# Kernel tuning notes

Hardware: AMD Instinct MI355X
Metric: run time of the kernel (lower is better)

The kernel has to match this reference:

```python
import jax, jax.numpy as jnp
import numpy as np

B, S, D, H = 4, 2048, 512, 8
DEPTH = D // H
EPS = 1e-6

def setup_inputs() -> dict:
    key = jax.random.key(0)
    ks = jax.random.split(key, 5)
    scale = 1.0 / np.sqrt(D)
    return {
        "x": jax.random.normal(ks[0], (B, S, D), dtype=jnp.float32),
        "wq": jax.random.normal(ks[1], (D, D), dtype=jnp.float32) * scale,
        "wk": jax.random.normal(ks[2], (D, D), dtype=jnp.float32) * scale,
        "wv": jax.random.normal(ks[3], (D, D), dtype=jnp.float32) * scale,
        "wo": jax.random.normal(ks[4], (D, D), dtype=jnp.float32) * scale,
        "bo": jnp.zeros((D,), dtype=jnp.float32),
        "gamma": jnp.ones((D,), dtype=jnp.float32),
        "beta": jnp.zeros((D,), dtype=jnp.float32),
    }

def _split_heads(t):
    # [B,S,D] -> [B,H,S,depth]
    return t.reshape(B, S, H, DEPTH).transpose(0, 2, 1, 3)

def reference(x, wq, wk, wv, wo, bo, gamma, beta):
    q = _split_heads(x @ wq)
    k = _split_heads(x @ wk)
    v = _split_heads(x @ wv)
    logits = jnp.einsum("bhqd,bhkd->bhqk", q, k) / jnp.sqrt(jnp.float32(DEPTH))
    attn = jax.nn.softmax(logits, axis=-1)  # dropout is identity at inference
    ctx = jnp.einsum("bhqk,bhkd->bhqd", attn, v)
    ctx = ctx.transpose(0, 2, 1, 3).reshape(B, S, D)
    out = ctx @ wo + bo
    resid = x + out  # output dropout identity at inference
    mu = jnp.mean(resid, axis=-1, keepdims=True)
    var = jnp.mean(jnp.square(resid - mu), axis=-1, keepdims=True)
    return (resid - mu) / jnp.sqrt(var + EPS) * gamma + beta
```

## Files before the change

### kernel.cpp

```cpp
#include <hip/hip_runtime.h>
#include <hip/hip_bf16.h>

typedef __attribute__((ext_vector_type(8))) short short8;
typedef __attribute__((ext_vector_type(4))) float f32x4;

constexpr int B_ = 4, S_ = 2048, D_ = 512, H_ = 8, DP_ = 64;
constexpr int M_ = B_ * S_;

__device__ __forceinline__ unsigned short f2b(float f) {
    __hip_bfloat16 h = __float2bfloat16(f);
    return *reinterpret_cast<unsigned short*>(&h);
}

__device__ __forceinline__ void gload_lds16(const unsigned short* g, unsigned short* l) {
    __builtin_amdgcn_global_load_lds((const __attribute__((address_space(1))) void*)g,
                                     (__attribute__((address_space(3))) void*)l, 16, 0, 0);
}

#define MFMA16(a, b, c) __builtin_amdgcn_mfma_f32_16x16x32_bf16((a), (b), (c), 0, 0, 0)
#define ASM_BAR() asm volatile("s_barrier" ::: "memory")

__global__ __launch_bounds__(256)
void prep(const float* __restrict__ x, unsigned short* __restrict__ xb,
          const float* __restrict__ w0, const float* __restrict__ w1,
          const float* __restrict__ w2, const float* __restrict__ w3,
          unsigned short* __restrict__ outw) {
    __shared__ float t[64][65];
    int bx = blockIdx.x;
    int tid = threadIdx.x;
    if (bx < 4096) {
        int i = bx * 256 + tid;
        float4 v = ((const float4*)x)[i];
        ushort4 o;
        o.x = f2b(v.x); o.y = f2b(v.y); o.z = f2b(v.z); o.w = f2b(v.w);
        ((ushort4*)xb)[i] = o;
        return;
    }
    int b = bx - 4096;
    int z = b >> 6, r = b & 63;
    int k0 = (r >> 3) * 64, n0 = (r & 7) * 64;
    const float* in = (z == 0) ? w0 : (z == 1) ? w1 : (z == 2) ? w2 : w3;
    unsigned short* out = outw + (size_t)z * D_ * D_;
    int tx = tid & 63, ty = tid >> 6;
#pragma unroll
    for (int i = 0; i < 16; i++) {
        int rr = ty * 16 + i;
        t[rr][tx] = in[(size_t)(k0 + rr) * D_ + n0 + tx];
    }
    __syncthreads();
#pragma unroll
    for (int i = 0; i < 16; i++) {
        int rr = ty * 16 + i;
        out[(size_t)(n0 + rr) * D_ + k0 + tx] = f2b(t[tx][rr]);
    }
}

__global__ __launch_bounds__(256, 3)
void gemm_qkvv(const unsigned short* __restrict__ X,
               const unsigned short* __restrict__ Wt,
               unsigned short* __restrict__ QKV,
               unsigned short* __restrict__ Vt) {
    int z = blockIdx.z;
    int tid = threadIdx.x;
    int wave = tid >> 6, lane = tid & 63, l16 = lane & 15, quad = lane >> 4;
    int wm = (wave >> 1) * 64, wn = (wave & 1) * 64;

    int m0, n0, bb = 0;
    const unsigned short *Abase, *Bbase;
    if (z < 2) {
        m0 = blockIdx.x * 128; n0 = blockIdx.y * 128;
        Abase = X + (size_t)m0 * D_;
        Bbase = Wt + (size_t)z * D_ * D_ + (size_t)n0 * D_;
    } else {
        int idx = blockIdx.y * 64 + blockIdx.x;
        bb = idx >> 6;
        int r = idx & 63;
        m0 = (r & 3) * 128;
        n0 = (r >> 2) * 128;
        Abase = Wt + 2 * (size_t)D_ * D_ + (size_t)m0 * D_;
        Bbase = X + ((size_t)bb * S_ + n0) * D_;
    }

    __shared__ __align__(16) unsigned short SM[17408];
    unsigned short (*As)[64] = reinterpret_cast<unsigned short(*)[64]>(SM);
    unsigned short (*Bs)[64] = reinterpret_cast<unsigned short(*)[64]>(SM + 8192);
    unsigned short (*Cs)[136] = reinterpret_cast<unsigned short(*)[136]>(SM);

    const int psw = l16 & 7;
    const int drow = lane >> 3;
    const int dsw = (lane & 7) ^ drow;

    f32x4 acc[4][4];
    const f32x4 zf = {0.f, 0.f, 0.f, 0.f};
#pragma unroll
    for (int i = 0; i < 4; i++)
#pragma unroll
        for (int j = 0; j < 4; j++) acc[i][j] = zf;

    for (int k0 = 0; k0 < D_; k0 += 64) {
        __syncthreads();
#pragma unroll
        for (int j = 0; j < 4; j++) {
            int r8 = wave * 32 + j * 8;
            gload_lds16(Abase + (size_t)(r8 + drow) * D_ + k0 + dsw * 8, &As[r8][0]);
            gload_lds16(Bbase + (size_t)(r8 + drow) * D_ + k0 + dsw * 8, &Bs[r8][0]);
        }
        __syncthreads();
#pragma unroll
        for (int h = 0; h < 2; h++) {
            short8 af[4], bf[4];
#pragma unroll
            for (int mt = 0; mt < 4; mt++)
                af[mt] = *(const short8*)&As[wm + mt * 16 + l16][((h * 4 + quad) ^ psw) * 8];
#pragma unroll
            for (int nt = 0; nt < 4; nt++)
                bf[nt] = *(const short8*)&Bs[wn + nt * 16 + l16][((h * 4 + quad) ^ psw) * 8];
#pragma unroll
            for (int nt = 0; nt < 4; nt++)
#pragma unroll
                for (int mt = 0; mt < 4; mt++)
                    acc[nt][mt] = MFMA16(bf[nt], af[mt], acc[nt][mt]);
        }
    }
    __syncthreads();
#pragma unroll
    for (int nt = 0; nt < 4; nt++)
#pragma unroll
        for (int mt = 0; mt < 4; mt++) {
            ushort4 pk;
            pk.x = f2b(acc[nt][mt][0]); pk.y = f2b(acc[nt][mt][1]);
            pk.z = f2b(acc[nt][mt][2]); pk.w = f2b(acc[nt][mt][3]);
            *(ushort4*)&Cs[wm + mt * 16 + l16][wn + nt * 16 + quad * 4] = pk;
        }
    __syncthreads();
    if (z < 2) {
        unsigned short* out = QKV + (size_t)z * M_ * D_;
#pragma unroll
        for (int i = 0; i < 8; i++) {
            int c = tid + i * 256;
            int ml = c >> 4, nch = c & 15;
            int m = m0 + ml, n = n0 + nch * 8;
            int b2 = m >> 11, ss = m & 2047, hh = n >> 6, dd = n & 63;
            *(short8*)(out + ((((size_t)b2 * H_ + hh) * S_ + ss) * DP_ + dd)) =
                *(const short8*)&Cs[ml][nch * 8];
        }
    } else {
#pragma unroll
        for (int i = 0; i < 8; i++) {
            int c = tid + i * 256;
            int ml = c >> 4, nch = c & 15;
            *(short8*)(Vt + ((size_t)bb * D_ + m0 + ml) * S_ + n0 + nch * 8) =
                *(const short8*)&Cs[ml][nch * 8];
        }
    }
}

__global__ __launch_bounds__(256, 3)
void flash_attn(const unsigned short* __restrict__ Qg, const unsigned short* __restrict__ Kg,
                const unsigned short* __restrict__ Vt, unsigned short* __restrict__ ctx) {
    int bid0 = blockIdx.x;
    int bid = (bid0 & 7) * 64 + (bid0 >> 3);
    int qt = bid & 15, hh = (bid >> 4) & 7, bb = bid >> 7;
    int tid = threadIdx.x;
    int wave = tid >> 6, lane = tid & 63, l16 = lane & 15, quad = lane >> 4;
    int qh = quad >> 1, ql = quad & 1;

    size_t bh = ((size_t)bb * H_ + hh) * S_ * DP_;
    const unsigned short* Qb = Qg + bh;
    const unsigned short* Kb = Kg + bh;
    const unsigned short* Vb = Vt + bh;

    __shared__ __align__(16) unsigned short Kls[2][64][64];
    __shared__ __align__(16) unsigned short Vls[2][64][64];
    __shared__ __align__(16) unsigned short Ps[4][32][64];

    const int psw = l16 & 7;
    const int drow = (lane >> 3) & 7;
    const int dsw = (lane & 7) ^ drow;

    short8 qa0, qa1, qb0, qb1;
    {
        const unsigned short* qp = Qb + (size_t)(qt * 128 + wave * 32 + l16) * DP_ + quad * 8;
        qa0 = *(const short8*)qp;
        qa1 = *(const short8*)(qp + 32);
        qb0 = *(const short8*)(qp + 16 * DP_);
        qb1 = *(const short8*)(qp + 16 * DP_ + 32);
    }

    auto stage = [&](int kv, int b) {
#pragma unroll
        for (int j = 0; j < 2; j++) {
            int r8 = (wave * 2 + j) * 8;
            int r = r8 + drow;
            gload_lds16(Kb + (size_t)(kv + r) * DP_ + dsw * 8, &Kls[b][r8][0]);
            gload_lds16(Vb + (size_t)r * S_ + kv + dsw * 8,    &Vls[b][r8][0]);
        }
    };

    stage(0, 0);
    stage(64, 1);
    asm volatile("s_waitcnt vmcnt(4)" ::: "memory");
    ASM_BAR();

    const f32x4 zf = {0.f, 0.f, 0.f, 0.f};
    f32x4 oa[4], ob[4];
#pragma unroll
    for (int i = 0; i < 4; i++) { oa[i] = zf; ob[i] = zf; }
    float m2a = -1e30f, m2b = -1e30f;
    float lsa = 0.f, lsb = 0.f;
    constexpr float c1 = 0.125f * 1.44269504088896f;

    int cur = 0;
    for (int t = 0; t < 32; t++) {
        __builtin_amdgcn_s_setprio(1);
        f32x4 sa[4], sb[4];
#pragma unroll
        for (int nt = 0; nt < 4; nt++) {
            const unsigned short* kr = &Kls[cur][nt * 16 + l16][0];
            short8 kf0 = *(const short8*)(kr + ((quad ^ psw) * 8));
            short8 kf1 = *(const short8*)(kr + (((quad ^ 4) ^ psw) * 8));
            f32x4 s = zf;
            s = MFMA16(kf0, qa0, s);
            s = MFMA16(kf1, qa1, s);
            sa[nt] = s;
            s = zf;
            s = MFMA16(kf0, qb0, s);
            s = MFMA16(kf1, qb1, s);
            sb[nt] = s;
        }
        __builtin_amdgcn_s_setprio(0);

        float ga, gb;
        {
            float ta[4], tb[4];
#pragma unroll
            for (int nt = 0; nt < 4; nt++) {
                ta[nt] = fmaxf(fmaxf(sa[nt][0], sa[nt][1]), fmaxf(sa[nt][2], sa[nt][3]));
                tb[nt] = fmaxf(fmaxf(sb[nt][0], sb[nt][1]), fmaxf(sb[nt][2], sb[nt][3]));
            }
            ga = fmaxf(fmaxf(ta[0], ta[1]), fmaxf(ta[2], ta[3]));
            gb = fmaxf(fmaxf(tb[0], tb[1]), fmaxf(tb[2], tb[3]));
        }
        ga = fmaxf(ga, __shfl_xor(ga, 16));
        ga = fmaxf(ga, __shfl_xor(ga, 32));
        gb = fmaxf(gb, __shfl_xor(gb, 16));
        gb = fmaxf(gb, __shfl_xor(gb, 32));
        ga *= c1; gb *= c1;
        float ala = 1.0f, alb = 1.0f;
        bool need = !__all((ga <= m2a + 8.0f) && (gb <= m2b + 8.0f));
        if (need) {
            float na = fmaxf(m2a, ga), nb = fmaxf(m2b, gb);
            ala = __builtin_amdgcn_exp2f(m2a - na);
            alb = __builtin_amdgcn_exp2f(m2b - nb);
            m2a = na; m2b = nb;
        }
        float rsa = 0.f, rsb = 0.f;
#pragma unroll
        for (int nt = 0; nt < 4; nt++) {
            float a0 = __builtin_amdgcn_exp2f(__builtin_fmaf(sa[nt][0], c1, -m2a));
            float a1 = __builtin_amdgcn_exp2f(__builtin_fmaf(sa[nt][1], c1, -m2a));
            float a2 = __builtin_amdgcn_exp2f(__builtin_fmaf(sa[nt][2], c1, -m2a));
            float a3 = __builtin_amdgcn_exp2f(__builtin_fmaf(sa[nt][3], c1, -m2a));
            rsa += (a0 + a1) + (a2 + a3);
            ushort4 pk;
            pk.x = f2b(a0); pk.y = f2b(a1); pk.z = f2b(a2); pk.w = f2b(a3);
            int c8 = (2 * nt + qh) ^ psw;
            *(ushort4*)&Ps[wave][l16][c8 * 8 + 4 * ql] = pk;
            float b0 = __builtin_amdgcn_exp2f(__builtin_fmaf(sb[nt][0], c1, -m2b));
            float b1 = __builtin_amdgcn_exp2f(__builtin_fmaf(sb[nt][1], c1, -m2b));
            float b2 = __builtin_amdgcn_exp2f(__builtin_fmaf(sb[nt][2], c1, -m2b));
            float b3 = __builtin_amdgcn_exp2f(__builtin_fmaf(sb[nt][3], c1, -m2b));
            rsb += (b0 + b1) + (b2 + b3);
            pk.x = f2b(b0); pk.y = f2b(b1); pk.z = f2b(b2); pk.w = f2b(b3);
            *(ushort4*)&Ps[wave][16 + l16][c8 * 8 + 4 * ql] = pk;
        }
        rsa += __shfl_xor(rsa, 16);
        rsa += __shfl_xor(rsa, 32);
        rsb += __shfl_xor(rsb, 16);
        rsb += __shfl_xor(rsb, 32);
        lsa = ala * lsa + rsa;
        lsb = alb * lsb + rsb;
        if (need) {
            float a0 = __shfl(ala, quad * 4 + 0), a1 = __shfl(ala, quad * 4 + 1);
            float a2 = __shfl(ala, quad * 4 + 2), a3 = __shfl(ala, quad * 4 + 3);
            float b0 = __shfl(alb, quad * 4 + 0), b1 = __shfl(alb, quad * 4 + 1);
            float b2 = __shfl(alb, quad * 4 + 2), b3 = __shfl(alb, quad * 4 + 3);
#pragma unroll
            for (int ot = 0; ot < 4; ot++) {
                oa[ot][0] *= a0; oa[ot][1] *= a1; oa[ot][2] *= a2; oa[ot][3] *= a3;
                ob[ot][0] *= b0; ob[ot][1] *= b1; ob[ot][2] *= b2; ob[ot][3] *= b3;
            }
        }

        __builtin_amdgcn_s_setprio(1);
#pragma unroll
        for (int kt = 0; kt < 2; kt++) {
            int pc = ((kt * 4 + quad) ^ psw) * 8;
            short8 pfA = *(const short8*)&Ps[wave][l16][pc];
            short8 pfB = *(const short8*)&Ps[wave][16 + l16][pc];
#pragma unroll
            for (int ot = 0; ot < 4; ot++) {
                short8 vf = *(const short8*)&Vls[cur][ot * 16 + l16][pc];
                oa[ot] = MFMA16(pfA, vf, oa[ot]);
                ob[ot] = MFMA16(pfB, vf, ob[ot]);
            }
        }
        __builtin_amdgcn_s_setprio(0);

        ASM_BAR();
        if (t < 30) {
            stage((t + 2) * 64, cur);
            asm volatile("s_waitcnt vmcnt(4)" ::: "memory");
        } else {
            asm volatile("s_waitcnt vmcnt(0)" ::: "memory");
        }
        ASM_BAR();
        cur ^= 1;
    }

    float la0 = __shfl(lsa, quad * 4 + 0), la1 = __shfl(lsa, quad * 4 + 1);
    float la2 = __shfl(lsa, quad * 4 + 2), la3 = __shfl(lsa, quad * 4 + 3);
    float lb0 = __shfl(lsb, quad * 4 + 0), lb1 = __shfl(lsb, quad * 4 + 1);
    float lb2 = __shfl(lsb, quad * 4 + 2), lb3 = __shfl(lsb, quad * 4 + 3);
    float ia0 = __builtin_amdgcn_rcpf(la0), ia1 = __builtin_amdgcn_rcpf(la1);
    float ia2 = __builtin_amdgcn_rcpf(la2), ia3 = __builtin_amdgcn_rcpf(la3);
    float ib0 = __builtin_amdgcn_rcpf(lb0), ib1 = __builtin_amdgcn_rcpf(lb1);
    float ib2 = __builtin_amdgcn_rcpf(lb2), ib3 = __builtin_amdgcn_rcpf(lb3);
    int srow0 = qt * 128 + wave * 32 + quad * 4;
#pragma unroll
    for (int ot = 0; ot < 4; ot++) {
        size_t base = ((size_t)bb * S_ + srow0) * D_ + hh * DP_ + ot * 16 + l16;
        ctx[base]          = f2b(oa[ot][0] * ia0);
        ctx[base + D_]     = f2b(oa[ot][1] * ia1);
        ctx[base + 2 * D_] = f2b(oa[ot][2] * ia2);
        ctx[base + 3 * D_] = f2b(oa[ot][3] * ia3);
        size_t baseB = base + (size_t)16 * D_;
        ctx[baseB]          = f2b(ob[ot][0] * ib0);
        ctx[baseB + D_]     = f2b(ob[ot][1] * ib1);
        ctx[baseB + 2 * D_] = f2b(ob[ot][2] * ib2);
        ctx[baseB + 3 * D_] = f2b(ob[ot][3] * ib3);
    }
}

__global__ __launch_bounds__(256, 3)
void gemm_proj(const unsigned short* __restrict__ A,
               const unsigned short* __restrict__ Bt,
               float* __restrict__ outf) {
    int m0 = blockIdx.x * 128, n0 = blockIdx.y * 128;
    int tid = threadIdx.x;
    int wave = tid >> 6, lane = tid & 63, l16 = lane & 15, quad = lane >> 4;
    int wm = (wave >> 1) * 64, wn = (wave & 1) * 64;

    __shared__ __align__(16) unsigned short As[128][64];
    __shared__ __align__(16) unsigned short Bs[128][64];

    const int psw = l16 & 7;
    const int drow = lane >> 3;
    const int dsw = (lane & 7) ^ drow;

    f32x4 acc[4][4];
    const f32x4 zf = {0.f, 0.f, 0.f, 0.f};
#pragma unroll
    for (int i = 0; i < 4; i++)
#pragma unroll
        for (int j = 0; j < 4; j++) acc[i][j] = zf;

    for (int k0 = 0; k0 < D_; k0 += 64) {
        __syncthreads();
#pragma unroll
        for (int j = 0; j < 4; j++) {
            int r8 = wave * 32 + j * 8;
            gload_lds16(A  + (size_t)(m0 + r8 + drow) * D_ + k0 + dsw * 8, &As[r8][0]);
            gload_lds16(Bt + (size_t)(n0 + r8 + drow) * D_ + k0 + dsw * 8, &Bs[r8][0]);
        }
        __syncthreads();
#pragma unroll
        for (int h = 0; h < 2; h++) {
            short8 af[4], bf[4];
#pragma unroll
            for (int mt = 0; mt < 4; mt++)
                af[mt] = *(const short8*)&As[wm + mt * 16 + l16][((h * 4 + quad) ^ psw) * 8];
#pragma unroll
            for (int nt = 0; nt < 4; nt++)
                bf[nt] = *(const short8*)&Bs[wn + nt * 16 + l16][((h * 4 + quad) ^ psw) * 8];
#pragma unroll
            for (int nt = 0; nt < 4; nt++)
#pragma unroll
                for (int mt = 0; mt < 4; mt++)
                    acc[nt][mt] = MFMA16(bf[nt], af[mt], acc[nt][mt]);
        }
    }
#pragma unroll
    for (int nt = 0; nt < 4; nt++)
#pragma unroll
        for (int mt = 0; mt < 4; mt++) {
            int m = m0 + wm + mt * 16 + l16;
            int n = n0 + wn + nt * 16 + quad * 4;
            *(f32x4*)&outf[(size_t)m * D_ + n] = acc[nt][mt];
        }
}

__global__ __launch_bounds__(256, 8)
void ln_out(const float* __restrict__ tmp, const float* __restrict__ Xg,
            const float* __restrict__ bo, const float* __restrict__ gamma,
            const float* __restrict__ beta, float* __restrict__ outp) {
    int wave = threadIdx.x >> 6, lane = threadIdx.x & 63;
    int row = blockIdx.x * 4 + wave;
    const float4* t4 = (const float4*)(tmp + (size_t)row * D_);
    const float4* x4 = (const float4*)(Xg + (size_t)row * D_);
    const float4* b4 = (const float4*)bo;
    const float4* g4 = (const float4*)gamma;
    const float4* e4 = (const float4*)beta;
    float4* o4 = (float4*)(outp + (size_t)row * D_);

    float4 r[2];
    float sum = 0.f, sq = 0.f;
#pragma unroll
    for (int i = 0; i < 2; i++) {
        int c = lane + i * 64;
        float4 a = t4[c], x = x4[c], b = b4[c];
        r[i].x = a.x + x.x + b.x;
        r[i].y = a.y + x.y + b.y;
        r[i].z = a.z + x.z + b.z;
        r[i].w = a.w + x.w + b.w;
        sum += (r[i].x + r[i].y) + (r[i].z + r[i].w);
        sq += (r[i].x * r[i].x + r[i].y * r[i].y) + (r[i].z * r[i].z + r[i].w * r[i].w);
    }
#pragma unroll
    for (int off = 1; off < 64; off <<= 1) {
        sum += __shfl_xor(sum, off);
        sq += __shfl_xor(sq, off);
    }
    float mu = sum * (1.0f / D_);
    float var = sq * (1.0f / D_) - mu * mu;
    float rstd = rsqrtf(var + 1e-6f);
#pragma unroll
    for (int i = 0; i < 2; i++) {
        int c = lane + i * 64;
        float4 g = g4[c], e = e4[c];
        float4 o;
        o.x = (r[i].x - mu) * rstd * g.x + e.x;
        o.y = (r[i].y - mu) * rstd * g.y + e.y;
        o.z = (r[i].z - mu) * rstd * g.z + e.z;
        o.w = (r[i].w - mu) * rstd * g.w + e.w;
        o4[c] = o;
    }
}

extern "C" void kernel_launch(void* const* d_in, const int* in_sizes, int n_in,
                              void* d_out, int out_size, void* d_ws, size_t ws_size,
                              hipStream_t stream) {
    const float* x     = (const float*)d_in[0];
    const float* wq    = (const float*)d_in[1];
    const float* wk    = (const float*)d_in[2];
    const float* wv    = (const float*)d_in[3];
    const float* wo    = (const float*)d_in[4];
    const float* bo    = (const float*)d_in[5];
    const float* gamma = (const float*)d_in[6];
    const float* beta  = (const float*)d_in[7];
    float* out = (float*)d_out;

    unsigned short* xb  = (unsigned short*)d_ws;
    unsigned short* wt  = xb + (size_t)M_ * D_;
    unsigned short* Q   = wt + 4 * D_ * D_;
    unsigned short* K   = Q + (size_t)M_ * D_;
    unsigned short* Vt  = K + (size_t)M_ * D_;
    unsigned short* ctx = xb;
    float* tmp = (float*)Q;

    prep<<<dim3(4096 + 256), 256, 0, stream>>>(x, xb, wq, wk, wv, wo, wt);
    gemm_qkvv<<<dim3(64, 4, 3), 256, 0, stream>>>(xb, wt, Q, Vt);
    flash_attn<<<dim3(512), 256, 0, stream>>>(Q, K, Vt, ctx);
    gemm_proj<<<dim3(64, 4), 256, 0, stream>>>(ctx, wt + 3 * (size_t)D_ * D_, tmp);
    ln_out<<<dim3(2048), 256, 0, stream>>>(tmp, x, bo, gamma, beta, out);
}
```

Measured before the change: 187.4 us.

## Double-buffer LDS tiles in QKV and projection GEMMs with async prefetch

Both GEMM kernels now keep two LDS stages and issue the global-to-LDS loads for tile t+2 while computing tile t, using explicit vmcnt waits and raw barriers instead of two __syncthreads per k-step. This is meant to hide global load latency behind MFMA work. LDS use doubles to 64KB per block and launch bounds drop from 3 to 2 blocks per CU, so there is less occupancy-based latency hiding.

```diff
diff --git a/kernel.cpp b/kernel.cpp
--- a/kernel.cpp
+++ b/kernel.cpp
@@ -55,7 +55,7 @@
     }
 }
 
-__global__ __launch_bounds__(256, 3)
+__global__ __launch_bounds__(256, 2)
 void gemm_qkvv(const unsigned short* __restrict__ X,
                const unsigned short* __restrict__ Wt,
                unsigned short* __restrict__ QKV,
@@ -81,15 +81,25 @@
         Bbase = X + ((size_t)bb * S_ + n0) * D_;
     }
 
-    __shared__ __align__(16) unsigned short SM[17408];
-    unsigned short (*As)[64] = reinterpret_cast<unsigned short(*)[64]>(SM);
-    unsigned short (*Bs)[64] = reinterpret_cast<unsigned short(*)[64]>(SM + 8192);
+    __shared__ __align__(16) unsigned short SM[32768];
     unsigned short (*Cs)[136] = reinterpret_cast<unsigned short(*)[136]>(SM);
 
     const int psw = l16 & 7;
     const int drow = lane >> 3;
     const int dsw = (lane & 7) ^ drow;
 
+    auto stage = [&](int t, int b) {
+        int k0 = t * 64;
+        unsigned short* As = SM + b * 16384;
+        unsigned short* Bs = SM + b * 16384 + 8192;
+#pragma unroll
+        for (int j = 0; j < 4; j++) {
+            int r8 = wave * 32 + j * 8;
+            gload_lds16(Abase + (size_t)(r8 + drow) * D_ + k0 + dsw * 8, As + r8 * 64);
+            gload_lds16(Bbase + (size_t)(r8 + drow) * D_ + k0 + dsw * 8, Bs + r8 * 64);
+        }
+    };
+
     f32x4 acc[4][4];
     const f32x4 zf = {0.f, 0.f, 0.f, 0.f};
 #pragma unroll
@@ -97,29 +107,39 @@
 #pragma unroll
         for (int j = 0; j < 4; j++) acc[i][j] = zf;
 
-    for (int k0 = 0; k0 < D_; k0 += 64) {
-        __syncthreads();
-#pragma unroll
-        for (int j = 0; j < 4; j++) {
-            int r8 = wave * 32 + j * 8;
-            gload_lds16(Abase + (size_t)(r8 + drow) * D_ + k0 + dsw * 8, &As[r8][0]);
-            gload_lds16(Bbase + (size_t)(r8 + drow) * D_ + k0 + dsw * 8, &Bs[r8][0]);
-        }
-        __syncthreads();
+    stage(0, 0);
+    stage(1, 1);
+    asm volatile("s_waitcnt vmcnt(8)" ::: "memory");
+    ASM_BAR();
+
+    for (int t = 0; t < 8; t++) {
+        int b = t & 1;
+        const unsigned short* As = SM + b * 16384;
+        const unsigned short* Bs = SM + b * 16384 + 8192;
 #pragma unroll
         for (int h = 0; h < 2; h++) {
             short8 af[4], bf[4];
 #pragma unroll
             for (int mt = 0; mt < 4; mt++)
-                af[mt] = *(const short8*)&As[wm + mt * 16 + l16][((h * 4 + quad) ^ psw) * 8];
+                af[mt] = *(const short8*)(As + (wm + mt * 16 + l16) * 64 + ((h * 4 + quad) ^ psw) * 8);
 #pragma unroll
             for (int nt = 0; nt < 4; nt++)
-                bf[nt] = *(const short8*)&Bs[wn + nt * 16 + l16][((h * 4 + quad) ^ psw) * 8];
+                bf[nt] = *(const short8*)(Bs + (wn + nt * 16 + l16) * 64 + ((h * 4 + quad) ^ psw) * 8);
 #pragma unroll
             for (int nt = 0; nt < 4; nt++)
 #pragma unroll
                 for (int mt = 0; mt < 4; mt++)
                     acc[nt][mt] = MFMA16(bf[nt], af[mt], acc[nt][mt]);
+        }
+        if (t < 7) {
+            ASM_BAR();
+            if (t < 6) {
+                stage(t + 2, b);
+                asm volatile("s_waitcnt vmcnt(8)" ::: "memory");
+            } else {
+                asm volatile("s_waitcnt vmcnt(0)" ::: "memory");
+            }
+            ASM_BAR();
         }
     }
     __syncthreads();
@@ -342,7 +362,7 @@
     }
 }
 
-__global__ __launch_bounds__(256, 3)
+__global__ __launch_bounds__(256, 2)
 void gemm_proj(const unsigned short* __restrict__ A,
                const unsigned short* __restrict__ Bt,
                float* __restrict__ outf) {
@@ -351,13 +371,27 @@
     int wave = tid >> 6, lane = tid & 63, l16 = lane & 15, quad = lane >> 4;
     int wm = (wave >> 1) * 64, wn = (wave & 1) * 64;
 
-    __shared__ __align__(16) unsigned short As[128][64];
-    __shared__ __align__(16) unsigned short Bs[128][64];
+    __shared__ __align__(16) unsigned short SM[32768];
 
     const int psw = l16 & 7;
     const int drow = lane >> 3;
     const int dsw = (lane & 7) ^ drow;
 
+    const unsigned short* Abase = A + (size_t)m0 * D_;
+    const unsigned short* Bbase = Bt + (size_t)n0 * D_;
+
+    auto stage = [&](int t, int b) {
+        int k0 = t * 64;
+        unsigned short* As = SM + b * 16384;
+        unsigned short* Bs = SM + b * 16384 + 8192;
+#pragma unroll
+        for (int j = 0; j < 4; j++) {
+            int r8 = wave * 32 + j * 8;
+            gload_lds16(Abase + (size_t)(r8 + drow) * D_ + k0 + dsw * 8, As + r8 * 64);
+            gload_lds16(Bbase + (size_t)(r8 + drow) * D_ + k0 + dsw * 8, Bs + r8 * 64);
+        }
+    };
+
     f32x4 acc[4][4];
     const f32x4 zf = {0.f, 0.f, 0.f, 0.f};
 #pragma unroll
@@ -365,29 +399,39 @@
 #pragma unroll
         for (int j = 0; j < 4; j++) acc[i][j] = zf;
 
-    for (int k0 = 0; k0 < D_; k0 += 64) {
-        __syncthreads();
-#pragma unroll
-        for (int j = 0; j < 4; j++) {
-            int r8 = wave * 32 + j * 8;
-            gload_lds16(A  + (size_t)(m0 + r8 + drow) * D_ + k0 + dsw * 8, &As[r8][0]);
-            gload_lds16(Bt + (size_t)(n0 + r8 + drow) * D_ + k0 + dsw * 8, &Bs[r8][0]);
-        }
-        __syncthreads();
+    stage(0, 0);
+    stage(1, 1);
+    asm volatile("s_waitcnt vmcnt(8)" ::: "memory");
+    ASM_BAR();
+
+    for (int t = 0; t < 8; t++) {
+        int b = t & 1;
+        const unsigned short* As = SM + b * 16384;
+        const unsigned short* Bs = SM + b * 16384 + 8192;
 #pragma unroll
         for (int h = 0; h < 2; h++) {
             short8 af[4], bf[4];
 #pragma unroll
             for (int mt = 0; mt < 4; mt++)
-                af[mt] = *(const short8*)&As[wm + mt * 16 + l16][((h * 4 + quad) ^ psw) * 8];
+                af[mt] = *(const short8*)(As + (wm + mt * 16 + l16) * 64 + ((h * 4 + quad) ^ psw) * 8);
 #pragma unroll
             for (int nt = 0; nt < 4; nt++)
-                bf[nt] = *(const short8*)&Bs[wn + nt * 16 + l16][((h * 4 + quad) ^ psw) * 8];
+                bf[nt] = *(const short8*)(Bs + (wn + nt * 16 + l16) * 64 + ((h * 4 + quad) ^ psw) * 8);
 #pragma unroll
             for (int nt = 0; nt < 4; nt++)
 #pragma unroll
                 for (int mt = 0; mt < 4; mt++)
                     acc[nt][mt] = MFMA16(bf[nt], af[mt], acc[nt][mt]);
+        }
+        if (t < 7) {
+            ASM_BAR();
+            if (t < 6) {
+                stage(t + 2, b);
+                asm volatile("s_waitcnt vmcnt(8)" ::: "memory");
+            } else {
+                asm volatile("s_waitcnt vmcnt(0)" ::: "memory");
+            }
+            ASM_BAR();
         }
     }
 #pragma unroll
```

After: 178.2 us. 4.9% less time.
